# Kernel optimization log

Hardware: AMD Instinct MI355X
Metric: run time of the kernel (lower is better)

The kernel has to match this reference:

```python
import jax, jax.numpy as jnp
import numpy as np

B, T, C = 2, 2048, 1024
N_HEAD = 16
HEAD_DIM = C // N_HEAD


def setup_inputs() -> dict:
    key = jax.random.key(0)
    k1, k2, k3 = jax.random.split(key, 3)
    x = jax.random.normal(k1, (B, T, C), dtype=jnp.float32)
    w_attn = jax.random.normal(k2, (C, 3 * C), dtype=jnp.float32) * 0.02
    b_attn = jnp.zeros((3 * C,), dtype=jnp.float32)
    w_proj = jax.random.normal(k3, (C, C), dtype=jnp.float32) * 0.02
    b_proj = jnp.zeros((C,), dtype=jnp.float32)
    return {"x": x, "w_attn": w_attn, "b_attn": b_attn, "w_proj": w_proj, "b_proj": b_proj}


def reference(x, w_attn, b_attn, w_proj, b_proj):
    Bz, Tz, Cz = x.shape
    qkv = x @ w_attn + b_attn                       # [B, T, 3C]
    q, k, v = jnp.split(qkv, 3, axis=-1)
    # [B, H, T, D]
    q = q.reshape(Bz, Tz, N_HEAD, HEAD_DIM).transpose(0, 2, 1, 3)
    k = k.reshape(Bz, Tz, N_HEAD, HEAD_DIM).transpose(0, 2, 1, 3)
    v = v.reshape(Bz, Tz, N_HEAD, HEAD_DIM).transpose(0, 2, 1, 3)
    scale = 1.0 / np.sqrt(HEAD_DIM).astype(np.float32)
    att = jnp.einsum('bhqd,bhkd->bhqk', q, k) * scale  # [B, H, T, T]
    causal = jnp.tril(jnp.ones((Tz, Tz), dtype=bool))
    att = jnp.where(causal[None, None], att, -jnp.inf)
    att = jax.nn.softmax(att, axis=-1)
    y = jnp.einsum('bhqk,bhkd->bhqd', att, v)          # [B, H, T, D]
    y = y.transpose(0, 2, 1, 3).reshape(Bz, Tz, Cz)
    return y @ w_proj + b_proj
```

## Files before the change

kernel.cpp:

```cpp
#include <hip/hip_runtime.h>
#include <stdint.h>

#define T_SEQ 2048
#define NH 16
#define HD 64
#define M_DIM 4096
#define K_DIM 1024

typedef __attribute__((ext_vector_type(8))) short bf16x8;
typedef __attribute__((ext_vector_type(4))) short bf16x4;
typedef __attribute__((ext_vector_type(4))) float f32x4;
typedef __attribute__((ext_vector_type(4))) unsigned short u16x4;

__device__ __forceinline__ unsigned short f2bf(float f) {
  union { float f; uint32_t u; } x; x.f = f;
  uint32_t u = x.u;
  return (unsigned short)((u + 0x7fffu + ((u >> 16) & 1u)) >> 16);
}

__device__ __forceinline__ uint32_t cvtpk_bf16(float a, float b) {
  uint32_t r;
  asm("v_cvt_pk_bf16_f32 %0, %1, %2" : "=v"(r) : "v"(a), "v"(b));
  return r;
}

__device__ __forceinline__ f32x4 mfma16(bf16x4 a, bf16x4 b, f32x4 c) {
  asm("v_mfma_f32_16x16x16_bf16 %0, %1, %2, %0" : "+v"(c) : "v"(a), "v"(b));
  return c;
}

__device__ __forceinline__ float max3f(float a, float b, float c) {
  return fmaxf(fmaxf(a, b), c);
}

#define GLOAD16(g, l) __builtin_amdgcn_global_load_lds( \
    (const __attribute__((address_space(1))) unsigned int*)(g), \
    (__attribute__((address_space(3))) unsigned int*)(l), 16, 0, 0)

__device__ __forceinline__ void do_convert(const float* __restrict__ src,
                                           unsigned short* __restrict__ dst, int bid) {
  int idx = (bid * 256 + threadIdx.x) * 4;
  f32x4 v = *(const f32x4*)(src + idx);
  u16x4 o;
  #pragma unroll
  for (int i = 0; i < 4; ++i) o[i] = f2bf(v[i]);
  *(u16x4*)(dst + idx) = o;
}

__device__ __forceinline__ void do_transpose(const float* __restrict__ src,
                                             unsigned short* __restrict__ dst,
                                             int R, int Cn, int bx, int by,
                                             float (*tile)[65]) {
  const int r0 = by * 64, c0 = bx * 64;
  const int t = threadIdx.x;
  const int rr = t >> 4;
  const int c4 = (t & 15) * 4;
  #pragma unroll
  for (int p = 0; p < 4; ++p) {
    f32x4 v = *(const f32x4*)(src + (size_t)(r0 + p * 16 + rr) * Cn + c0 + c4);
    #pragma unroll
    for (int i = 0; i < 4; ++i) tile[p * 16 + rr][c4 + i] = v[i];
  }
  __syncthreads();
  #pragma unroll
  for (int p = 0; p < 4; ++p) {
    const int cl = p * 16 + rr;
    u16x4 o;
    #pragma unroll
    for (int i = 0; i < 4; ++i) o[i] = f2bf(tile[c4 + i][cl]);
    *(u16x4*)(dst + (size_t)(c0 + cl) * R + r0 + c4) = o;
  }
}

__global__ __launch_bounds__(256) void prep_kernel(
    const float* __restrict__ x, unsigned short* __restrict__ xb,
    const float* __restrict__ w_attn, unsigned short* __restrict__ wqkvT,
    const float* __restrict__ w_proj, unsigned short* __restrict__ wprojT) {
  __shared__ float tile[64][65];
  const int b = blockIdx.x;
  if (b < 4096) {
    do_convert(x, xb, b);
  } else if (b < 4096 + 768) {
    const int bid = b - 4096;
    do_transpose(w_attn, wqkvT, 1024, 3072, bid % 48, bid / 48, tile);
  } else {
    const int bid = b - 4864;
    do_transpose(w_proj, wprojT, 1024, 1024, bid % 16, bid / 16, tile);
  }
}

template <int MODE>
__global__ __launch_bounds__(256, 3) void gemm3_kernel(
    const unsigned short* __restrict__ A,
    const unsigned short* __restrict__ Bt,
    const float* __restrict__ bias,
    unsigned short* __restrict__ qout,
    unsigned short* __restrict__ kout,
    unsigned short* __restrict__ vTout,
    float* __restrict__ fout) {
  constexpr int NS = K_DIM / 32;
  constexpr int NWG = (MODE == 0) ? 768 : 256;
  constexpr int NBC = (MODE == 0) ? 24 : 8;
  __shared__ __align__(16) unsigned short As[3][128 * 32];
  __shared__ __align__(16) unsigned short Bs[3][128 * 32];
  const int t = threadIdx.x;
  const int w = t >> 6, l = t & 63;
  const int wr = w >> 1, wc = w & 1;
  const int lr = l & 15, lg = l >> 4;
  const int wg = (blockIdx.x & 7) * (NWG >> 3) + (blockIdx.x >> 3);
  const int bc = wg % NBC, br = wg / NBC;

  f32x4 acc[4][4];
  const f32x4 zf = {0.f, 0.f, 0.f, 0.f};
  #pragma unroll
  for (int i = 0; i < 4; ++i)
    #pragma unroll
    for (int j = 0; j < 4; ++j) acc[i][j] = zf;

  const unsigned short* Abase = A + (size_t)(br * 128) * K_DIM;
  const unsigned short* Bbase = Bt + (size_t)(bc * 128) * K_DIM;
  const int uA0 = t, uA1 = t + 256;
  const int uB0 = t, uB1 = t + 256;

  #define STAGE(ks, buf) do {                                                   \
    const int k0 = (ks) * 32;                                                   \
    unsigned short* as = &As[0][0] + (buf) * (128 * 32);                        \
    unsigned short* bs = &Bs[0][0] + (buf) * (128 * 32);                        \
    GLOAD16(Abase + (size_t)(uA0 >> 2) * K_DIM + k0 + (uA0 & 3) * 8, as + uA0 * 8); \
    GLOAD16(Abase + (size_t)(uA1 >> 2) * K_DIM + k0 + (uA1 & 3) * 8, as + uA1 * 8); \
    GLOAD16(Bbase + (size_t)(uB0 >> 2) * K_DIM + k0 + (uB0 & 3) * 8, bs + uB0 * 8); \
    GLOAD16(Bbase + (size_t)(uB1 >> 2) * K_DIM + k0 + (uB1 & 3) * 8, bs + uB1 * 8); \
  } while (0)

  #define COMPUTE(buf) do {                                                      \
    const unsigned short* as = &As[0][0] + (buf) * (128 * 32);                   \
    const unsigned short* bs = &Bs[0][0] + (buf) * (128 * 32);                   \
    bf16x8 af[4], bfv[4];                                                        \
    _Pragma("unroll")                                                            \
    for (int f = 0; f < 4; ++f) {                                                \
      af[f]  = *(const bf16x8*)(as + (wr * 64 + f * 16 + lr) * 32 + lg * 8);     \
      bfv[f] = *(const bf16x8*)(bs + (wc * 64 + f * 16 + lr) * 32 + lg * 8);     \
    }                                                                            \
    _Pragma("unroll")                                                            \
    for (int fr = 0; fr < 4; ++fr)                                               \
      _Pragma("unroll")                                                          \
      for (int fc = 0; fc < 4; ++fc)                                             \
        acc[fr][fc] = __builtin_amdgcn_mfma_f32_16x16x32_bf16(af[fr], bfv[fc],   \
                                                              acc[fr][fc], 0, 0, 0); \
  } while (0)

  STAGE(0, 0);
  STAGE(1, 1);
  int b_cur = 0;
  #pragma unroll 1
  for (int ks = 0; ks < NS; ++ks) {
    if (ks == NS - 1) {
      asm volatile("s_waitcnt vmcnt(0)" ::: "memory");
    } else {
      asm volatile("s_waitcnt vmcnt(4)" ::: "memory");
    }
    __builtin_amdgcn_sched_barrier(0);
    __builtin_amdgcn_s_barrier();
    if (ks + 2 < NS) {
      const int b_stg = (b_cur == 0) ? 2 : b_cur - 1;
      STAGE(ks + 2, b_stg);
    }
    COMPUTE(b_cur);
    b_cur = (b_cur == 2) ? 0 : b_cur + 1;
  }
  #undef STAGE
  #undef COMPUTE

  #pragma unroll
  for (int fr = 0; fr < 4; ++fr) {
    #pragma unroll
    for (int fc = 0; fc < 4; ++fc) {
      const int m0 = br * 128 + wr * 64 + fr * 16 + lg * 4;
      const int n  = bc * 128 + wc * 64 + fc * 16 + lr;
      if (MODE == 0) {
        const int which = n >> 10, rem = n & 1023;
        const int h = rem >> 6, d = rem & 63;
        const int b = m0 >> 11, tt0 = m0 & 2047;
        const int bh = b * NH + h;
        if (which == 2) {
          u16x4 pack;
          #pragma unroll
          for (int r = 0; r < 4; ++r) pack[r] = f2bf(acc[fr][fc][r] + bias[n]);
          *(u16x4*)(vTout + ((size_t)bh * HD + d) * T_SEQ + tt0) = pack;
        } else {
          unsigned short* o = (which == 0) ? qout : kout;
          const float sc = (which == 0) ? 0.18033688011112042f : 1.0f;
          #pragma unroll
          for (int r = 0; r < 4; ++r)
            o[((size_t)bh * T_SEQ + tt0 + r) * HD + d] = f2bf((acc[fr][fc][r] + bias[n]) * sc);
        }
      } else {
        #pragma unroll
        for (int r = 0; r < 4; ++r)
          fout[(size_t)(m0 + r) * 1024 + n] = acc[fr][fc][r] + bias[n];
      }
    }
  }
}

__global__ __launch_bounds__(256, 3) void flash_attn_kernel(
    const unsigned short* __restrict__ qg,
    const unsigned short* __restrict__ kg,
    const unsigned short* __restrict__ vTg,
    unsigned short* __restrict__ yg) {
  __shared__ __align__(16) unsigned short Ks[3][64 * 64];
  __shared__ __align__(16) unsigned short Vs[3][64 * 64];

  const int t = threadIdx.x;
  const int w = t >> 6, l = t & 63;
  const int lr = l & 15, lg = l >> 4;
  const int i = blockIdx.x;
  const int bh = (i & 7) * 4 + ((i >> 3) & 3);
  const int qt = 31 - (i >> 5);
  const int nt = qt + 1;
  const int qw = qt * 64 + w * 16;
  const int qrow = qw + lr;
  const int swz = lr & 7;

  const int srow0 = t >> 3;
  const int sch = t & 7;

  const size_t kgb = (size_t)bh * T_SEQ * HD;
  const size_t vgb = (size_t)bh * HD * T_SEQ;
  const f32x4 zf = {0.f, 0.f, 0.f, 0.f};

  const size_t qoff = ((size_t)bh * T_SEQ + qw + lr) * HD + lg * 8;
  const bf16x8 qf0 = *(const bf16x8*)(qg + qoff);
  const bf16x8 qf1 = *(const bf16x8*)(qg + qoff + 32);

  f32x4 acc[4];
  #pragma unroll
  for (int k = 0; k < 4; ++k) acc[k] = zf;
  float m_run = 0.f;
  float l_part = 0.f;
  bool rescaled = false;

  #define FSTAGE(kvt, buf) do {                                                  \
    const size_t kof = kgb + (size_t)(kvt) * 64 * HD;                            \
    const size_t vof = vgb + (size_t)(kvt) * 64;                                 \
    _Pragma("unroll")                                                            \
    for (int sh = 0; sh < 2; ++sh) {                                             \
      const int row = sh * 32 + srow0;                                           \
      const int sc = (sch ^ (row & 7)) * 8;                                      \
      GLOAD16(kg + kof + (size_t)row * HD + sc, Ks[buf] + row * 64 + sch * 8);   \
      GLOAD16(vTg + vof + (size_t)row * T_SEQ + sc, Vs[buf] + row * 64 + sch * 8); \
    }                                                                            \
  } while (0)

  FSTAGE(0, 0);
  if (nt > 1) FSTAGE(1, 1);

  int cur = 0;
  #pragma unroll 1
  for (int it = 0; it < nt; ++it) {
    if (it == nt - 1) {
      asm volatile("s_waitcnt vmcnt(0)" ::: "memory");
    } else {
      asm volatile("s_waitcnt vmcnt(4)" ::: "memory");
    }
    __builtin_amdgcn_sched_barrier(0);
    __builtin_amdgcn_s_barrier();
    if (it + 2 < nt) {
      const int b_stg = (cur == 0) ? 2 : cur - 1;
      FSTAGE(it + 2, b_stg);
    }

    const int kv0 = it * 64;
    f32x4 s[4];
    __builtin_amdgcn_s_setprio(1);
    #pragma unroll
    for (int fc = 0; fc < 4; ++fc) {
      const unsigned short* kr = Ks[cur] + (fc * 16 + lr) * 64;
      const bf16x8 k0v = *(const bf16x8*)(kr + ((lg ^ swz) * 8));
      const bf16x8 k1v = *(const bf16x8*)(kr + (((lg + 4) ^ swz) * 8));
      f32x4 sv = zf;
      sv = __builtin_amdgcn_mfma_f32_16x16x32_bf16(k0v, qf0, sv, 0, 0, 0);
      sv = __builtin_amdgcn_mfma_f32_16x16x32_bf16(k1v, qf1, sv, 0, 0, 0);
      s[fc] = sv;
    }
    __builtin_amdgcn_s_setprio(0);

    if (it == nt - 1) {
      #pragma unroll
      for (int fc = 0; fc < 4; ++fc)
        #pragma unroll
        for (int r = 0; r < 4; ++r) {
          const int tkv = kv0 + fc * 16 + lg * 4 + r;
          if (tkv > qrow) s[fc][r] = -1e30f;
        }
    }

    float mt = max3f(s[0][0], s[0][1], s[0][2]);
    mt = max3f(mt, s[0][3], s[1][0]);
    mt = max3f(mt, s[1][1], s[1][2]);
    mt = max3f(mt, s[1][3], s[2][0]);
    mt = max3f(mt, s[2][1], s[2][2]);
    mt = max3f(mt, s[2][3], s[3][0]);
    mt = max3f(mt, s[3][1], s[3][2]);
    mt = fmaxf(mt, s[3][3]);
    if (__any(mt > m_run + 8.f)) {
      float mrow = fmaxf(mt, __shfl_xor(mt, 16));
      mrow = fmaxf(mrow, __shfl_xor(mrow, 32));
      const float m_new = fmaxf(m_run, mrow);
      const float fac = __builtin_amdgcn_exp2f(m_run - m_new);
      l_part *= fac;
      float frs[4];
      #pragma unroll
      for (int r = 0; r < 4; ++r) frs[r] = __shfl(fac, lg * 4 + r);
      #pragma unroll
      for (int fd = 0; fd < 4; ++fd)
        #pragma unroll
        for (int r = 0; r < 4; ++r) acc[fd][r] *= frs[r];
      m_run = m_new;
      rescaled = true;
    }

    float e[4][4];
    if (rescaled) {
      #pragma unroll
      for (int fc = 0; fc < 4; ++fc)
        #pragma unroll
        for (int r = 0; r < 4; ++r)
          e[fc][r] = __builtin_amdgcn_exp2f(s[fc][r] - m_run);
    } else {
      #pragma unroll
      for (int fc = 0; fc < 4; ++fc)
        #pragma unroll
        for (int r = 0; r < 4; ++r)
          e[fc][r] = __builtin_amdgcn_exp2f(s[fc][r]);
    }
    union { uint32_t d[2]; bf16x4 v; } pkd[4];
    #pragma unroll
    for (int fc = 0; fc < 4; ++fc) {
      pkd[fc].d[0] = cvtpk_bf16(e[fc][0], e[fc][1]);
      pkd[fc].d[1] = cvtpk_bf16(e[fc][2], e[fc][3]);
    }
    l_part += (((e[0][0] + e[0][1]) + (e[0][2] + e[0][3])) +
               ((e[1][0] + e[1][1]) + (e[1][2] + e[1][3]))) +
              (((e[2][0] + e[2][1]) + (e[2][2] + e[2][3])) +
               ((e[3][0] + e[3][1]) + (e[3][2] + e[3][3])));

    __builtin_amdgcn_s_setprio(1);
    #pragma unroll
    for (int fd = 0; fd < 4; ++fd) {
      const unsigned short* vr = Vs[cur] + (fd * 16 + lr) * 64;
      bf16x4 vf[4];
      #pragma unroll
      for (int fc = 0; fc < 4; ++fc) {
        const int ch = (fc * 2 + (lg >> 1)) ^ swz;
        vf[fc] = *(const bf16x4*)(vr + ch * 8 + (lg & 1) * 4);
      }
      f32x4 a = acc[fd];
      #pragma unroll
      for (int fc = 0; fc < 4; ++fc) a = mfma16(pkd[fc].v, vf[fc], a);
      acc[fd] = a;
    }
    __builtin_amdgcn_s_setprio(0);
    cur = (cur == 2) ? 0 : cur + 1;
  }
  #undef FSTAGE

  float lsum = l_part;
  lsum += __shfl_xor(lsum, 16);
  lsum += __shfl_xor(lsum, 32);

  const int b = bh >> 4, h = bh & 15;
  #pragma unroll
  for (int r = 0; r < 4; ++r) {
    const float lv = __shfl(lsum, lg * 4 + r);
    const float linv = 1.f / lv;
    const int tt = qw + lg * 4 + r;
    #pragma unroll
    for (int fd = 0; fd < 4; ++fd) {
      const int d = fd * 16 + lr;
      yg[(((size_t)b * T_SEQ + tt) * NH + h) * HD + d] = f2bf(acc[fd][r] * linv);
    }
  }
}

extern "C" void kernel_launch(void* const* d_in, const int* in_sizes, int n_in,
                              void* d_out, int out_size, void* d_ws, size_t ws_size,
                              hipStream_t stream) {
  (void)in_sizes; (void)n_in; (void)out_size; (void)ws_size;
  const float* x      = (const float*)d_in[0];
  const float* w_attn = (const float*)d_in[1];
  const float* b_attn = (const float*)d_in[2];
  const float* w_proj = (const float*)d_in[3];
  const float* b_proj = (const float*)d_in[4];
  float* out = (float*)d_out;

  char* ws = (char*)d_ws;
  unsigned short* xb     = (unsigned short*)(ws);
  unsigned short* wqkvT  = (unsigned short*)(ws + (8ull  << 20));
  unsigned short* wprojT = (unsigned short*)(ws + (14ull << 20));
  unsigned short* qb     = (unsigned short*)(ws + (16ull << 20));
  unsigned short* kb     = (unsigned short*)(ws + (24ull << 20));
  unsigned short* vT     = (unsigned short*)(ws + (32ull << 20));
  unsigned short* yb     = (unsigned short*)(ws + (40ull << 20));

  prep_kernel<<<5120, 256, 0, stream>>>(x, xb, w_attn, wqkvT, w_proj, wprojT);
  gemm3_kernel<0><<<768, 256, 0, stream>>>(xb, wqkvT, b_attn, qb, kb, vT, nullptr);
  flash_attn_kernel<<<1024, 256, 0, stream>>>(qb, kb, vT, yb);
  gemm3_kernel<1><<<256, 256, 0, stream>>>(yb, wprojT, b_proj, nullptr, nullptr, nullptr, out);
}
```

Baseline: 180.6 us.

## Process 128 query rows per attention block to reuse K/V tiles across two fragments

Each flash-attention block now handles a 128-row query tile, with every wave owning two 16-row fragments (A and B) that share the K and V tiles loaded into LDS. This halves the grid to 512 blocks and halves K/V global-to-LDS traffic per query row. The schedule pairs tiles g and 15-g across the two grid halves to balance causal work. The cost is more registers (occupancy bound lowered from 3 to 2 blocks) and fewer blocks, so latency hiding and load balance may suffer.

```diff
diff --git a/kernel.cpp b/kernel.cpp
--- a/kernel.cpp
+++ b/kernel.cpp
@@ -203,7 +203,7 @@
   }
 }
 
-__global__ __launch_bounds__(256, 3) void flash_attn_kernel(
+__global__ __launch_bounds__(256, 2) void flash_attn_kernel(
     const unsigned short* __restrict__ qg,
     const unsigned short* __restrict__ kg,
     const unsigned short* __restrict__ vTg,
@@ -215,11 +215,13 @@
   const int w = t >> 6, l = t & 63;
   const int lr = l & 15, lg = l >> 4;
   const int i = blockIdx.x;
-  const int bh = (i & 7) * 4 + ((i >> 3) & 3);
-  const int qt = 31 - (i >> 5);
-  const int nt = qt + 1;
-  const int qw = qt * 64 + w * 16;
-  const int qrow = qw + lr;
+  const int half = i >> 8, j = i & 255;
+  const int bh = (j & 7) * 4 + ((j >> 3) & 3);
+  const int g = j >> 5;
+  const int qt = half ? g : (15 - g);
+  const int nt = 2 * qt + 2;
+  const int qw = qt * 128 + w * 32;
+  const int qrowA = qw + lr, qrowB = qw + 16 + lr;
   const int swz = lr & 7;
 
   const int srow0 = t >> 3;
@@ -229,15 +231,17 @@
   const size_t vgb = (size_t)bh * HD * T_SEQ;
   const f32x4 zf = {0.f, 0.f, 0.f, 0.f};
 
-  const size_t qoff = ((size_t)bh * T_SEQ + qw + lr) * HD + lg * 8;
-  const bf16x8 qf0 = *(const bf16x8*)(qg + qoff);
-  const bf16x8 qf1 = *(const bf16x8*)(qg + qoff + 32);
-
-  f32x4 acc[4];
-  #pragma unroll
-  for (int k = 0; k < 4; ++k) acc[k] = zf;
-  float m_run = 0.f;
-  float l_part = 0.f;
+  const size_t qoffA = ((size_t)bh * T_SEQ + qw + lr) * HD + lg * 8;
+  const bf16x8 qfA0 = *(const bf16x8*)(qg + qoffA);
+  const bf16x8 qfA1 = *(const bf16x8*)(qg + qoffA + 32);
+  const bf16x8 qfB0 = *(const bf16x8*)(qg + qoffA + 16 * HD);
+  const bf16x8 qfB1 = *(const bf16x8*)(qg + qoffA + 16 * HD + 32);
+
+  f32x4 accA[4], accB[4];
+  #pragma unroll
+  for (int k = 0; k < 4; ++k) { accA[k] = zf; accB[k] = zf; }
+  float mA = 0.f, mB = 0.f;
+  float lA = 0.f, lB = 0.f;
   bool rescaled = false;
 
   #define FSTAGE(kvt, buf) do {                                                  \
@@ -253,7 +257,7 @@
   } while (0)
 
   FSTAGE(0, 0);
-  if (nt > 1) FSTAGE(1, 1);
+  FSTAGE(1, 1);
 
   int cur = 0;
   #pragma unroll 1
@@ -271,7 +275,7 @@
     }
 
     const int kv0 = it * 64;
-    f32x4 s[4];
+    f32x4 sA[4], sB[4];
     __builtin_amdgcn_s_setprio(1);
     #pragma unroll
     for (int fc = 0; fc < 4; ++fc) {
@@ -279,71 +283,116 @@
       const bf16x8 k0v = *(const bf16x8*)(kr + ((lg ^ swz) * 8));
       const bf16x8 k1v = *(const bf16x8*)(kr + (((lg + 4) ^ swz) * 8));
       f32x4 sv = zf;
-      sv = __builtin_amdgcn_mfma_f32_16x16x32_bf16(k0v, qf0, sv, 0, 0, 0);
-      sv = __builtin_amdgcn_mfma_f32_16x16x32_bf16(k1v, qf1, sv, 0, 0, 0);
-      s[fc] = sv;
+      sv = __builtin_amdgcn_mfma_f32_16x16x32_bf16(k0v, qfA0, sv, 0, 0, 0);
+      sv = __builtin_amdgcn_mfma_f32_16x16x32_bf16(k1v, qfA1, sv, 0, 0, 0);
+      sA[fc] = sv;
+      f32x4 sw = zf;
+      sw = __builtin_amdgcn_mfma_f32_16x16x32_bf16(k0v, qfB0, sw, 0, 0, 0);
+      sw = __builtin_amdgcn_mfma_f32_16x16x32_bf16(k1v, qfB1, sw, 0, 0, 0);
+      sB[fc] = sw;
     }
     __builtin_amdgcn_s_setprio(0);
 
-    if (it == nt - 1) {
+    if (it >= nt - 2) {
       #pragma unroll
       for (int fc = 0; fc < 4; ++fc)
         #pragma unroll
         for (int r = 0; r < 4; ++r) {
           const int tkv = kv0 + fc * 16 + lg * 4 + r;
-          if (tkv > qrow) s[fc][r] = -1e30f;
+          if (tkv > qrowA) sA[fc][r] = -1e30f;
+          if (tkv > qrowB) sB[fc][r] = -1e30f;
         }
     }
 
-    float mt = max3f(s[0][0], s[0][1], s[0][2]);
-    mt = max3f(mt, s[0][3], s[1][0]);
-    mt = max3f(mt, s[1][1], s[1][2]);
-    mt = max3f(mt, s[1][3], s[2][0]);
-    mt = max3f(mt, s[2][1], s[2][2]);
-    mt = max3f(mt, s[2][3], s[3][0]);
-    mt = max3f(mt, s[3][1], s[3][2]);
-    mt = fmaxf(mt, s[3][3]);
-    if (__any(mt > m_run + 8.f)) {
-      float mrow = fmaxf(mt, __shfl_xor(mt, 16));
-      mrow = fmaxf(mrow, __shfl_xor(mrow, 32));
-      const float m_new = fmaxf(m_run, mrow);
-      const float fac = __builtin_amdgcn_exp2f(m_run - m_new);
-      l_part *= fac;
-      float frs[4];
-      #pragma unroll
-      for (int r = 0; r < 4; ++r) frs[r] = __shfl(fac, lg * 4 + r);
+    float mtA = max3f(sA[0][0], sA[0][1], sA[0][2]);
+    mtA = max3f(mtA, sA[0][3], sA[1][0]);
+    mtA = max3f(mtA, sA[1][1], sA[1][2]);
+    mtA = max3f(mtA, sA[1][3], sA[2][0]);
+    mtA = max3f(mtA, sA[2][1], sA[2][2]);
+    mtA = max3f(mtA, sA[2][3], sA[3][0]);
+    mtA = max3f(mtA, sA[3][1], sA[3][2]);
+    mtA = fmaxf(mtA, sA[3][3]);
+    float mtB = max3f(sB[0][0], sB[0][1], sB[0][2]);
+    mtB = max3f(mtB, sB[0][3], sB[1][0]);
+    mtB = max3f(mtB, sB[1][1], sB[1][2]);
+    mtB = max3f(mtB, sB[1][3], sB[2][0]);
+    mtB = max3f(mtB, sB[2][1], sB[2][2]);
+    mtB = max3f(mtB, sB[2][3], sB[3][0]);
+    mtB = max3f(mtB, sB[3][1], sB[3][2]);
+    mtB = fmaxf(mtB, sB[3][3]);
+    if (__any(fmaxf(mtA - mA, mtB - mB) > 8.f)) {
+      float mrA = fmaxf(mtA, __shfl_xor(mtA, 16));
+      mrA = fmaxf(mrA, __shfl_xor(mrA, 32));
+      float mrB = fmaxf(mtB, __shfl_xor(mtB, 16));
+      mrB = fmaxf(mrB, __shfl_xor(mrB, 32));
+      const float mnA = fmaxf(mA, mrA), mnB = fmaxf(mB, mrB);
+      const float facA = __builtin_amdgcn_exp2f(mA - mnA);
+      const float facB = __builtin_amdgcn_exp2f(mB - mnB);
+      lA *= facA; lB *= facB;
+      float frsA[4], frsB[4];
+      #pragma unroll
+      for (int r = 0; r < 4; ++r) {
+        frsA[r] = __shfl(facA, lg * 4 + r);
+        frsB[r] = __shfl(facB, lg * 4 + r);
+      }
       #pragma unroll
       for (int fd = 0; fd < 4; ++fd)
         #pragma unroll
-        for (int r = 0; r < 4; ++r) acc[fd][r] *= frs[r];
-      m_run = m_new;
+        for (int r = 0; r < 4; ++r) {
+          accA[fd][r] *= frsA[r];
+          accB[fd][r] *= frsB[r];
+        }
+      mA = mnA; mB = mnB;
       rescaled = true;
     }
 
-    float e[4][4];
-    if (rescaled) {
-      #pragma unroll
-      for (int fc = 0; fc < 4; ++fc)
-        #pragma unroll
-        for (int r = 0; r < 4; ++r)
-          e[fc][r] = __builtin_amdgcn_exp2f(s[fc][r] - m_run);
-    } else {
-      #pragma unroll
-      for (int fc = 0; fc < 4; ++fc)
-        #pragma unroll
-        for (int r = 0; r < 4; ++r)
-          e[fc][r] = __builtin_amdgcn_exp2f(s[fc][r]);
-    }
-    union { uint32_t d[2]; bf16x4 v; } pkd[4];
-    #pragma unroll
-    for (int fc = 0; fc < 4; ++fc) {
-      pkd[fc].d[0] = cvtpk_bf16(e[fc][0], e[fc][1]);
-      pkd[fc].d[1] = cvtpk_bf16(e[fc][2], e[fc][3]);
-    }
-    l_part += (((e[0][0] + e[0][1]) + (e[0][2] + e[0][3])) +
-               ((e[1][0] + e[1][1]) + (e[1][2] + e[1][3]))) +
-              (((e[2][0] + e[2][1]) + (e[2][2] + e[2][3])) +
-               ((e[3][0] + e[3][1]) + (e[3][2] + e[3][3])));
+    union { uint32_t d[2]; bf16x4 v; } pkdA[4], pkdB[4];
+    {
+      float e[4][4];
+      if (rescaled) {
+        #pragma unroll
+        for (int fc = 0; fc < 4; ++fc)
+          #pragma unroll
+          for (int r = 0; r < 4; ++r) e[fc][r] = __builtin_amdgcn_exp2f(sA[fc][r] - mA);
+      } else {
+        #pragma unroll
+        for (int fc = 0; fc < 4; ++fc)
+          #pragma unroll
+          for (int r = 0; r < 4; ++r) e[fc][r] = __builtin_amdgcn_exp2f(sA[fc][r]);
+      }
+      #pragma unroll
+      for (int fc = 0; fc < 4; ++fc) {
+        pkdA[fc].d[0] = cvtpk_bf16(e[fc][0], e[fc][1]);
+        pkdA[fc].d[1] = cvtpk_bf16(e[fc][2], e[fc][3]);
+      }
+      lA += (((e[0][0] + e[0][1]) + (e[0][2] + e[0][3])) +
+             ((e[1][0] + e[1][1]) + (e[1][2] + e[1][3]))) +
+            (((e[2][0] + e[2][1]) + (e[2][2] + e[2][3])) +
+             ((e[3][0] + e[3][1]) + (e[3][2] + e[3][3])));
+    }
+    {
+      float e[4][4];
+      if (rescaled) {
+        #pragma unroll
+        for (int fc = 0; fc < 4; ++fc)
+          #pragma unroll
+          for (int r = 0; r < 4; ++r) e[fc][r] = __builtin_amdgcn_exp2f(sB[fc][r] - mB);
+      } else {
+        #pragma unroll
+        for (int fc = 0; fc < 4; ++fc)
+          #pragma unroll
+          for (int r = 0; r < 4; ++r) e[fc][r] = __builtin_amdgcn_exp2f(sB[fc][r]);
+      }
+      #pragma unroll
+      for (int fc = 0; fc < 4; ++fc) {
+        pkdB[fc].d[0] = cvtpk_bf16(e[fc][0], e[fc][1]);
+        pkdB[fc].d[1] = cvtpk_bf16(e[fc][2], e[fc][3]);
+      }
+      lB += (((e[0][0] + e[0][1]) + (e[0][2] + e[0][3])) +
+             ((e[1][0] + e[1][1]) + (e[1][2] + e[1][3]))) +
+            (((e[2][0] + e[2][1]) + (e[2][2] + e[2][3])) +
+             ((e[3][0] + e[3][1]) + (e[3][2] + e[3][3])));
+    }
 
     __builtin_amdgcn_s_setprio(1);
     #pragma unroll
@@ -355,30 +404,37 @@
         const int ch = (fc * 2 + (lg >> 1)) ^ swz;
         vf[fc] = *(const bf16x4*)(vr + ch * 8 + (lg & 1) * 4);
       }
-      f32x4 a = acc[fd];
-      #pragma unroll
-      for (int fc = 0; fc < 4; ++fc) a = mfma16(pkd[fc].v, vf[fc], a);
-      acc[fd] = a;
+      f32x4 a = accA[fd], b = accB[fd];
+      #pragma unroll
+      for (int fc = 0; fc < 4; ++fc) {
+        a = mfma16(pkdA[fc].v, vf[fc], a);
+        b = mfma16(pkdB[fc].v, vf[fc], b);
+      }
+      accA[fd] = a; accB[fd] = b;
     }
     __builtin_amdgcn_s_setprio(0);
     cur = (cur == 2) ? 0 : cur + 1;
   }
   #undef FSTAGE
 
-  float lsum = l_part;
-  lsum += __shfl_xor(lsum, 16);
-  lsum += __shfl_xor(lsum, 32);
+  float lsA = lA, lsB = lB;
+  lsA += __shfl_xor(lsA, 16);
+  lsA += __shfl_xor(lsA, 32);
+  lsB += __shfl_xor(lsB, 16);
+  lsB += __shfl_xor(lsB, 32);
 
   const int b = bh >> 4, h = bh & 15;
   #pragma unroll
   for (int r = 0; r < 4; ++r) {
-    const float lv = __shfl(lsum, lg * 4 + r);
-    const float linv = 1.f / lv;
-    const int tt = qw + lg * 4 + r;
+    const float lvA = __shfl(lsA, lg * 4 + r);
+    const float lvB = __shfl(lsB, lg * 4 + r);
+    const float liA = 1.f / lvA, liB = 1.f / lvB;
+    const int ttA = qw + lg * 4 + r;
     #pragma unroll
     for (int fd = 0; fd < 4; ++fd) {
       const int d = fd * 16 + lr;
-      yg[(((size_t)b * T_SEQ + tt) * NH + h) * HD + d] = f2bf(acc[fd][r] * linv);
+      yg[(((size_t)b * T_SEQ + ttA) * NH + h) * HD + d] = f2bf(accA[fd][r] * liA);
+      yg[(((size_t)b * T_SEQ + ttA + 16) * NH + h) * HD + d] = f2bf(accB[fd][r] * liB);
     }
   }
 }
@@ -405,6 +461,6 @@
 
   prep_kernel<<<5120, 256, 0, stream>>>(x, xb, w_attn, wqkvT, w_proj, wprojT);
   gemm3_kernel<0><<<768, 256, 0, stream>>>(xb, wqkvT, b_attn, qb, kb, vT, nullptr);
-  flash_attn_kernel<<<1024, 256, 0, stream>>>(qb, kb, vT, yb);
+  flash_attn_kernel<<<512, 256, 0, stream>>>(qb, kb, vT, yb);
   gemm3_kernel<1><<<256, 256, 0, stream>>>(yb, wprojT, b_proj, nullptr, nullptr, nullptr, out);
 }
```

New measurement: 190.4 us. 5.4% more time.
